# Optimization experiments

Measured on AMD Instinct MI355X. Metric: run time of the kernel, lower is better.

Reference implementation:

```python
import jax, jax.numpy as jnp
import numpy as np

EPS = 1e-6

def _log_g(x):
    # log of continuous g(x) = where(x>=0, x+0.5, sigmoid(x)) from minGRU paper
    return jnp.where(x >= 0, jnp.log(jax.nn.relu(x) + 0.5), -jax.nn.softplus(-x))

def setup_inputs() -> dict:
    key = jax.random.key(0)
    ks = jax.random.split(key, 4)
    B, S, D, E = 4, 2048, 1024, 8
    scale = D ** -0.5
    return {
        "inputs": jax.random.normal(ks[0], (B, S, D), dtype=jnp.float32),
        "norm_weight": jnp.ones((D,), jnp.float32),
        "router_w": jax.random.normal(ks[1], (E, D), jnp.float32) * scale,
        "router_b": jnp.zeros((E,), jnp.float32),
        "w_hg": jax.random.normal(ks[2], (E, 2 * D, D), jnp.float32) * scale,
        "w_out": jax.random.normal(ks[3], (E, D, D), jnp.float32) * scale,
    }

def reference(inputs, norm_weight, router_w, router_b, w_hg, w_out):
    D = inputs.shape[-1]
    # --- RMSNorm ---
    x = inputs * jax.lax.rsqrt(jnp.mean(inputs * inputs, axis=-1, keepdims=True) + EPS) * norm_weight
    # --- SMEAR: per-sample soft merge of expert weights via mean-pooled routing ---
    probs = jax.nn.softmax(jnp.mean(x, axis=1) @ router_w.T + router_b, axis=-1)  # [B,E]
    W_hg = jnp.einsum('be,ekd->bkd', probs, w_hg)    # [B,2D,D] merged to_hidden_and_gate
    W_out = jnp.einsum('be,eod->bod', probs, w_out)  # [B,D,D]  merged to_out
    # --- minGRU with merged weights (log-space parallel scan, no initial state) ---
    hg = jnp.einsum('bsd,bkd->bsk', x, W_hg)         # [B,S,2D]
    hidden, gate = hg[..., :D], hg[..., D:]
    log_coeffs = -jax.nn.softplus(gate)                      # log(1 - z_t)
    log_values = -jax.nn.softplus(-gate) + _log_g(hidden)    # log z_t + log g(h~_t)
    a_star = jnp.cumsum(log_coeffs, axis=1)
    log_h = a_star + jax.lax.cumlogsumexp(log_values - a_star, axis=1)
    h = jnp.exp(log_h)                               # [B,S,D] recurrent states
    new_state = h[:, -1:]                            # [B,1,D]
    out = jnp.einsum('bsk,bok->bso', h, W_out)       # proj_out
    aux_loss = jnp.zeros((), inputs.dtype)
    return (out + inputs, new_state, aux_loss)
```

## Files before the change

kernel.cpp:

```cpp
#include <hip/hip_runtime.h>
#include <hip/hip_bf16.h>
#include <hip/hip_fp16.h>

#define B_  4
#define S_  2048
#define D_  1024
#define E_  8
#define K2_ 2048

#define CHUNKS 64
#define CLEN   32

typedef __attribute__((ext_vector_type(8))) short short8;
typedef __attribute__((ext_vector_type(4))) float floatx4;

__device__ __forceinline__ void gld16(const void* g, const void* l) {
    __builtin_amdgcn_global_load_lds(
        (const __attribute__((address_space(1))) unsigned int*)g,
        (__attribute__((address_space(3))) unsigned int*)l, 16, 0, 0);
}

__device__ __forceinline__ unsigned short f2bf(float f) {
    unsigned int u = __float_as_uint(f);
    u += 0x7fffu + ((u >> 16) & 1u);
    return (unsigned short)(u >> 16);
}

__global__ void rmsnorm_k(const float* __restrict__ in, const float* __restrict__ nw,
                          __hip_bfloat16* __restrict__ x) {
    int b = blockIdx.y, s = blockIdx.x, t = threadIdx.x;
    const float4* row = (const float4*)(in + ((size_t)b * S_ + s) * D_);
    float4 v = row[t];
    float ss = v.x * v.x + v.y * v.y + v.z * v.z + v.w * v.w;
#pragma unroll
    for (int o = 32; o > 0; o >>= 1) ss += __shfl_down(ss, o, 64);
    __shared__ float ls[4];
    if ((t & 63) == 0) ls[t >> 6] = ss;
    __syncthreads();
    float tot = ls[0] + ls[1] + ls[2] + ls[3];
    float rs = rsqrtf(tot * (1.0f / (float)D_) + 1e-6f);
    float4 w = ((const float4*)nw)[t];
    ushort4 o;
    o.x = f2bf(v.x * rs * w.x); o.y = f2bf(v.y * rs * w.y);
    o.z = f2bf(v.z * rs * w.z); o.w = f2bf(v.w * rs * w.w);
    ((ushort4*)(x + ((size_t)b * S_ + s) * D_))[t] = o;
}

__global__ void xsum_k(const __hip_bfloat16* __restrict__ x, float* __restrict__ xs) {
    int d = blockIdx.x * 256 + threadIdx.x;
    int b = blockIdx.y;
    int s0 = blockIdx.z * 128;
    const __hip_bfloat16* p = x + ((size_t)b * S_ + s0) * D_ + d;
    float acc = 0.0f;
#pragma unroll 4
    for (int s = 0; s < 128; s++) { acc += __bfloat162float(*p); p += D_; }
    atomicAdd(&xs[b * D_ + d], acc);
}

__global__ void router_k(const float* __restrict__ xs, const float* __restrict__ rw,
                         const float* __restrict__ rb, float* __restrict__ probs,
                         float* __restrict__ aux) {
    int t = threadIdx.x;
    if (t == 255) *aux = 0.0f;
    int pair = t >> 3, sub = t & 7;
    int b = pair >> 3, e = pair & 7;
    float acc = 0.0f;
    for (int d = sub; d < D_; d += 8) acc += xs[b * D_ + d] * rw[e * D_ + d];
#pragma unroll
    for (int o = 4; o > 0; o >>= 1) acc += __shfl_down(acc, o, 8);
    __shared__ float lg[32];
    if (sub == 0) lg[pair] = acc * (1.0f / (float)S_) + rb[e];
    __syncthreads();
    if (t < 4) {
        float m = -1e30f;
        for (int e2 = 0; e2 < 8; e2++) m = fmaxf(m, lg[t * 8 + e2]);
        float ssum = 0.0f; float ex[8];
        for (int e2 = 0; e2 < 8; e2++) { ex[e2] = expf(lg[t * 8 + e2] - m); ssum += ex[e2]; }
        for (int e2 = 0; e2 < 8; e2++) probs[t * 8 + e2] = ex[e2] / ssum;
    }
}

__global__ void mix_k(const float* __restrict__ probs, const float* __restrict__ whg_e,
                      const float* __restrict__ wout_e, __hip_bfloat16* __restrict__ Whg,
                      __hip_bfloat16* __restrict__ Wout) {
    __shared__ float P[32];
    int t = threadIdx.x;
    if (t < 32) P[t] = probs[t];
    __syncthreads();
    size_t i4 = (size_t)blockIdx.x * 256 + t;
    const size_t T1q = (size_t)K2_ * D_ / 4;
    const size_t T2q = (size_t)D_ * D_ / 4;
    float4 a0 = {0,0,0,0}, a1 = {0,0,0,0}, a2 = {0,0,0,0}, a3 = {0,0,0,0};
    if (i4 < T1q) {
        const float4* src = (const float4*)whg_e;
#pragma unroll
        for (int e = 0; e < 8; e++) {
            float4 wv = src[(size_t)e * T1q + i4];
            float p0 = P[e], p1 = P[8 + e], p2 = P[16 + e], p3 = P[24 + e];
            a0.x += p0 * wv.x; a0.y += p0 * wv.y; a0.z += p0 * wv.z; a0.w += p0 * wv.w;
            a1.x += p1 * wv.x; a1.y += p1 * wv.y; a1.z += p1 * wv.z; a1.w += p1 * wv.w;
            a2.x += p2 * wv.x; a2.y += p2 * wv.y; a2.z += p2 * wv.z; a2.w += p2 * wv.w;
            a3.x += p3 * wv.x; a3.y += p3 * wv.y; a3.z += p3 * wv.z; a3.w += p3 * wv.w;
        }
        ushort4* dst = (ushort4*)Whg;
        ushort4 o;
        o.x = f2bf(a0.x); o.y = f2bf(a0.y); o.z = f2bf(a0.z); o.w = f2bf(a0.w);
        dst[0 * T1q + i4] = o;
        o.x = f2bf(a1.x); o.y = f2bf(a1.y); o.z = f2bf(a1.z); o.w = f2bf(a1.w);
        dst[1 * T1q + i4] = o;
        o.x = f2bf(a2.x); o.y = f2bf(a2.y); o.z = f2bf(a2.z); o.w = f2bf(a2.w);
        dst[2 * T1q + i4] = o;
        o.x = f2bf(a3.x); o.y = f2bf(a3.y); o.z = f2bf(a3.z); o.w = f2bf(a3.w);
        dst[3 * T1q + i4] = o;
    } else {
        size_t j4 = i4 - T1q;
        const float4* src = (const float4*)wout_e;
#pragma unroll
        for (int e = 0; e < 8; e++) {
            float4 wv = src[(size_t)e * T2q + j4];
            float p0 = P[e], p1 = P[8 + e], p2 = P[16 + e], p3 = P[24 + e];
            a0.x += p0 * wv.x; a0.y += p0 * wv.y; a0.z += p0 * wv.z; a0.w += p0 * wv.w;
            a1.x += p1 * wv.x; a1.y += p1 * wv.y; a1.z += p1 * wv.z; a1.w += p1 * wv.w;
            a2.x += p2 * wv.x; a2.y += p2 * wv.y; a2.z += p2 * wv.z; a2.w += p2 * wv.w;
            a3.x += p3 * wv.x; a3.y += p3 * wv.y; a3.z += p3 * wv.z; a3.w += p3 * wv.w;
        }
        ushort4* dst = (ushort4*)Wout;
        ushort4 o;
        o.x = f2bf(a0.x); o.y = f2bf(a0.y); o.z = f2bf(a0.z); o.w = f2bf(a0.w);
        dst[0 * T2q + j4] = o;
        o.x = f2bf(a1.x); o.y = f2bf(a1.y); o.z = f2bf(a1.z); o.w = f2bf(a1.w);
        dst[1 * T2q + j4] = o;
        o.x = f2bf(a2.x); o.y = f2bf(a2.y); o.z = f2bf(a2.z); o.w = f2bf(a2.w);
        dst[2 * T2q + j4] = o;
        o.x = f2bf(a3.x); o.y = f2bf(a3.y); o.z = f2bf(a3.z); o.w = f2bf(a3.w);
        dst[3 * T2q + j4] = o;
    }
}

__global__ __launch_bounds__(256) void gemm_hg_cv(
    const __hip_bfloat16* __restrict__ A, const __hip_bfloat16* __restrict__ Bm,
    __half2* __restrict__ cv) {
    const int K = D_;
    int bz = blockIdx.z;
    A  += (size_t)bz * S_ * D_;
    Bm += (size_t)bz * K2_ * D_;
    __half2* CV = cv + (size_t)bz * S_ * D_;
    int m0 = blockIdx.y * 128, n0 = blockIdx.x * 64;
    __shared__ __hip_bfloat16 lA[128][64];
    __shared__ __hip_bfloat16 lBh[64][64];
    __shared__ __hip_bfloat16 lBg[64][64];
    int t = threadIdx.x;
    int w = t >> 6, lane = t & 63;
    int lm = lane & 15, quad = lane >> 4;
    int wr = w >> 1, wc = w & 1;
    floatx4 acch[4][2] = {};
    floatx4 accg[4][2] = {};
    int srow = lane >> 3;
    int swzb = ((lane & 7) ^ srow) * 16;

    const __hip_bfloat16* Bh = Bm;
    const __hip_bfloat16* Bg = Bm + (size_t)D_ * K;

    for (int k0 = 0; k0 < K; k0 += 64) {
#pragma unroll
        for (int it = 0; it < 4; it++) {
            int r0 = (w * 4 + it) * 8;
            gld16((const char*)(A + (size_t)(m0 + r0 + srow) * K + k0) + swzb,
                  &lA[r0][0]);
        }
#pragma unroll
        for (int it = 0; it < 2; it++) {
            int r0 = (w * 2 + it) * 8;
            gld16((const char*)(Bh + (size_t)(n0 + r0 + srow) * K + k0) + swzb,
                  &lBh[r0][0]);
            gld16((const char*)(Bg + (size_t)(n0 + r0 + srow) * K + k0) + swzb,
                  &lBg[r0][0]);
        }
        __syncthreads();
#pragma unroll
        for (int kk = 0; kk < 64; kk += 32) {
            short8 af[4], bh[2], bg[2];
            int p = (((kk >> 3) + quad) ^ (lm & 7)) * 8;
#pragma unroll
            for (int i = 0; i < 4; i++)
                af[i] = *(const short8*)(&lA[wr * 64 + i * 16 + lm][p]);
#pragma unroll
            for (int j = 0; j < 2; j++) {
                bh[j] = *(const short8*)(&lBh[wc * 32 + j * 16 + lm][p]);
                bg[j] = *(const short8*)(&lBg[wc * 32 + j * 16 + lm][p]);
            }
#pragma unroll
            for (int i = 0; i < 4; i++)
#pragma unroll
                for (int j = 0; j < 2; j++) {
                    acch[i][j] = __builtin_amdgcn_mfma_f32_16x16x32_bf16(
                        af[i], bh[j], acch[i][j], 0, 0, 0);
                    accg[i][j] = __builtin_amdgcn_mfma_f32_16x16x32_bf16(
                        af[i], bg[j], accg[i][j], 0, 0, 0);
                }
        }
        __syncthreads();
    }
#pragma unroll
    for (int i = 0; i < 4; i++) {
#pragma unroll
        for (int j = 0; j < 2; j++) {
#pragma unroll
            for (int r = 0; r < 4; r++) {
                int m = m0 + wr * 64 + i * 16 + quad * 4 + r;
                int n = n0 + wc * 32 + j * 16 + lm;
                float hid = acch[i][j][r];
                float g   = accg[i][j][r];
                float c  = 1.0f / (1.0f + expf(g));
                float sg = 1.0f / (1.0f + expf(-g));
                float gfn = (hid >= 0.0f) ? (hid + 0.5f)
                                          : (1.0f / (1.0f + expf(-hid)));
                CV[(size_t)m * D_ + n] = __floats2half2_rn(c, sg * gfn);
            }
        }
    }
}

#define TM 128
#define TN 128
#define TBK 64
__global__ __launch_bounds__(256) void gemm_bf16_bt(
    const __hip_bfloat16* __restrict__ A, const __hip_bfloat16* __restrict__ Bm,
    float* __restrict__ C, const float* __restrict__ R,
    int M, int N, int K, size_t sa, size_t sb, size_t sc, size_t sr) {
    int bz = blockIdx.z;
    A += (size_t)bz * sa; Bm += (size_t)bz * sb; C += (size_t)bz * sc;
    if (R) R += (size_t)bz * sr;
    int m0 = blockIdx.y * TM, n0 = blockIdx.x * TN;
    __shared__ __hip_bfloat16 lA[TM][TBK];
    __shared__ __hip_bfloat16 lB[TN][TBK];
    int t = threadIdx.x;
    int w = t >> 6, lane = t & 63;
    int lm = lane & 15, quad = lane >> 4;
    int wr = w >> 1, wc = w & 1;
    floatx4 acc[4][4] = {};
    int srow = lane >> 3;
    int swzb = ((lane & 7) ^ srow) * 16;

    for (int k0 = 0; k0 < K; k0 += TBK) {
#pragma unroll
        for (int it = 0; it < 4; it++) {
            int r0 = (w * 4 + it) * 8;
            gld16((const char*)(A + (size_t)(m0 + r0 + srow) * K + k0) + swzb,
                  &lA[r0][0]);
            gld16((const char*)(Bm + (size_t)(n0 + r0 + srow) * K + k0) + swzb,
                  &lB[r0][0]);
        }
        __syncthreads();
#pragma unroll
        for (int kk = 0; kk < TBK; kk += 32) {
            short8 af[4], bf[4];
            int p = (((kk >> 3) + quad) ^ (lm & 7)) * 8;
#pragma unroll
            for (int i = 0; i < 4; i++)
                af[i] = *(const short8*)(&lA[wr * 64 + i * 16 + lm][p]);
#pragma unroll
            for (int j = 0; j < 4; j++)
                bf[j] = *(const short8*)(&lB[wc * 64 + j * 16 + lm][p]);
#pragma unroll
            for (int i = 0; i < 4; i++)
#pragma unroll
                for (int j = 0; j < 4; j++)
                    acc[i][j] = __builtin_amdgcn_mfma_f32_16x16x32_bf16(
                        af[i], bf[j], acc[i][j], 0, 0, 0);
        }
        __syncthreads();
    }
#pragma unroll
    for (int i = 0; i < 4; i++) {
#pragma unroll
        for (int j = 0; j < 4; j++) {
#pragma unroll
            for (int r = 0; r < 4; r++) {
                int m = m0 + wr * 64 + i * 16 + quad * 4 + r;
                int n = n0 + wc * 64 + j * 16 + lm;
                float v = acc[i][j][r];
                if (R) v += R[(size_t)m * N + n];
                C[(size_t)m * N + n] = v;
            }
        }
    }
}

__global__ void scanA_k(const __half2* __restrict__ cv, float* __restrict__ Cc,
                        float* __restrict__ Vc) {
    int c = blockIdx.x, b = blockIdx.y, t = threadIdx.x;
    const float4* p = (const float4*)(cv + (size_t)(b * S_ + c * CLEN) * D_) + t;
    float P0 = 1, P1 = 1, P2 = 1, P3 = 1;
    float V0 = 0, V1 = 0, V2 = 0, V3 = 0;
#pragma unroll 4
    for (int s = 0; s < CLEN; s++) {
        float4 raw = p[(size_t)s * (D_ / 4)];
        const __half2* e = (const __half2*)&raw;
        float c0 = __low2float(e[0]), v0 = __high2float(e[0]);
        float c1 = __low2float(e[1]), v1 = __high2float(e[1]);
        float c2 = __low2float(e[2]), v2 = __high2float(e[2]);
        float c3 = __low2float(e[3]), v3 = __high2float(e[3]);
        P0 *= c0; V0 = fmaf(c0, V0, v0);
        P1 *= c1; V1 = fmaf(c1, V1, v1);
        P2 *= c2; V2 = fmaf(c2, V2, v2);
        P3 *= c3; V3 = fmaf(c3, V3, v3);
    }
    size_t q = ((size_t)(b * CHUNKS + c)) * (D_ / 4) + t;
    ((float4*)Cc)[q] = make_float4(P0, P1, P2, P3);
    ((float4*)Vc)[q] = make_float4(V0, V1, V2, V3);
}

__global__ void scanC_k(const __half2* __restrict__ cv, const float* __restrict__ Cc,
                        const float* __restrict__ Vc,
                        __hip_bfloat16* __restrict__ hout, float* __restrict__ ns) {
    int c = blockIdx.x, b = blockIdx.y, t = threadIdx.x;
    float h0 = 0, h1 = 0, h2 = 0, h3 = 0;
#pragma unroll 4
    for (int cc = 0; cc < c; cc++) {
        size_t q = ((size_t)(b * CHUNKS + cc)) * (D_ / 4) + t;
        float4 C4 = ((const float4*)Cc)[q];
        float4 V4 = ((const float4*)Vc)[q];
        h0 = fmaf(C4.x, h0, V4.x); h1 = fmaf(C4.y, h1, V4.y);
        h2 = fmaf(C4.z, h2, V4.z); h3 = fmaf(C4.w, h3, V4.w);
    }
    const float4* p = (const float4*)(cv + (size_t)(b * S_ + c * CLEN) * D_) + t;
    ushort4* hq = (ushort4*)(hout + (size_t)(b * S_ + c * CLEN) * D_) + t;
#pragma unroll 4
    for (int s = 0; s < CLEN; s++) {
        float4 raw = p[(size_t)s * (D_ / 4)];
        const __half2* e = (const __half2*)&raw;
        h0 = fmaf(__low2float(e[0]), h0, __high2float(e[0]));
        h1 = fmaf(__low2float(e[1]), h1, __high2float(e[1]));
        h2 = fmaf(__low2float(e[2]), h2, __high2float(e[2]));
        h3 = fmaf(__low2float(e[3]), h3, __high2float(e[3]));
        ushort4 o;
        o.x = f2bf(h0); o.y = f2bf(h1); o.z = f2bf(h2); o.w = f2bf(h3);
        hq[(size_t)s * (D_ / 4)] = o;
    }
    if (c == CHUNKS - 1)
        ((float4*)(ns + (size_t)b * D_))[t] = make_float4(h0, h1, h2, h3);
}

extern "C" void kernel_launch(void* const* d_in, const int* in_sizes, int n_in,
                              void* d_out_v, int out_size, void* d_ws, size_t ws_size,
                              hipStream_t stream) {
    const float* inputs = (const float*)d_in[0];
    const float* nw     = (const float*)d_in[1];
    const float* rw     = (const float*)d_in[2];
    const float* rb     = (const float*)d_in[3];
    const float* whg_e  = (const float*)d_in[4];
    const float* wout_e = (const float*)d_in[5];
    float* out = (float*)d_out_v;

    float* ws = (float*)d_ws;
    __half2*        cv      = (__half2*)ws;
    __hip_bfloat16* x_bf    = (__hip_bfloat16*)(ws + 8388608);
    __hip_bfloat16* h_bf    = (__hip_bfloat16*)(ws + 12582912);
    __hip_bfloat16* Whg_bf  = (__hip_bfloat16*)(ws + 16777216);
    __hip_bfloat16* Wout_bf = (__hip_bfloat16*)(ws + 20971520);
    float* xsum  = ws + 23068672;
    float* probs = ws + 23072768;
    float* Cc    = ws + 23072800;
    float* Vc    = ws + 23334944;

    hipMemsetAsync(xsum, 0, (size_t)B_ * D_ * sizeof(float), stream);

    rmsnorm_k<<<dim3(S_, B_), 256, 0, stream>>>(inputs, nw, x_bf);
    xsum_k<<<dim3(D_ / 256, B_, 16), 256, 0, stream>>>(x_bf, xsum);
    router_k<<<1, 256, 0, stream>>>(xsum, rw, rb, probs,
                                    out + (size_t)B_ * S_ * D_ + (size_t)B_ * D_);
    mix_k<<<3072, 256, 0, stream>>>(probs, whg_e, wout_e, Whg_bf, Wout_bf);

    gemm_hg_cv<<<dim3(D_ / 64, S_ / 128, B_), 256, 0, stream>>>(x_bf, Whg_bf, cv);

    scanA_k<<<dim3(CHUNKS, B_), 256, 0, stream>>>(cv, Cc, Vc);
    scanC_k<<<dim3(CHUNKS, B_), 256, 0, stream>>>(
        cv, Cc, Vc, h_bf, out + (size_t)B_ * S_ * D_);

    gemm_bf16_bt<<<dim3(D_ / TN, S_ / TM, B_), 256, 0, stream>>>(
        h_bf, Wout_bf, out, inputs, S_, D_, D_,
        (size_t)S_ * D_, (size_t)D_ * D_, (size_t)S_ * D_, (size_t)S_ * D_);
}
```

Before: 334.2 us.

## Double-buffer LDS tiles in both GEMMs to overlap global loads with MFMA

```diff
diff --git a/kernel.cpp b/kernel.cpp
--- a/kernel.cpp
+++ b/kernel.cpp
@@ -65,6 +65,7 @@
     int pair = t >> 3, sub = t & 7;
     int b = pair >> 3, e = pair & 7;
     float acc = 0.0f;
+#pragma unroll 8
     for (int d = sub; d < D_; d += 8) acc += xs[b * D_ + d] * rw[e * D_ + d];
 #pragma unroll
     for (int o = 4; o > 0; o >>= 1) acc += __shfl_down(acc, o, 8);
@@ -146,9 +147,9 @@
     Bm += (size_t)bz * K2_ * D_;
     __half2* CV = cv + (size_t)bz * S_ * D_;
     int m0 = blockIdx.y * 128, n0 = blockIdx.x * 64;
-    __shared__ __hip_bfloat16 lA[128][64];
-    __shared__ __hip_bfloat16 lBh[64][64];
-    __shared__ __hip_bfloat16 lBg[64][64];
+    __shared__ __hip_bfloat16 lA[2][128][64];
+    __shared__ __hip_bfloat16 lBh[2][64][64];
+    __shared__ __hip_bfloat16 lBg[2][64][64];
     int t = threadIdx.x;
     int w = t >> 6, lane = t & 63;
     int lm = lane & 15, quad = lane >> 4;
@@ -161,33 +162,44 @@
     const __hip_bfloat16* Bh = Bm;
     const __hip_bfloat16* Bg = Bm + (size_t)D_ * K;
 
-    for (int k0 = 0; k0 < K; k0 += 64) {
+    auto stage = [&](int bb, int k0) {
 #pragma unroll
         for (int it = 0; it < 4; it++) {
             int r0 = (w * 4 + it) * 8;
             gld16((const char*)(A + (size_t)(m0 + r0 + srow) * K + k0) + swzb,
-                  &lA[r0][0]);
+                  &lA[bb][r0][0]);
         }
 #pragma unroll
         for (int it = 0; it < 2; it++) {
             int r0 = (w * 2 + it) * 8;
             gld16((const char*)(Bh + (size_t)(n0 + r0 + srow) * K + k0) + swzb,
-                  &lBh[r0][0]);
+                  &lBh[bb][r0][0]);
             gld16((const char*)(Bg + (size_t)(n0 + r0 + srow) * K + k0) + swzb,
-                  &lBg[r0][0]);
-        }
-        __syncthreads();
+                  &lBg[bb][r0][0]);
+        }
+    };
+
+    stage(0, 0);
+    int cur = 0;
+    for (int k0 = 0; k0 < K; k0 += 64) {
+        if (k0 + 64 < K) {
+            stage(cur ^ 1, k0 + 64);
+            asm volatile("s_waitcnt vmcnt(8)" ::: "memory");
+        } else {
+            asm volatile("s_waitcnt vmcnt(0)" ::: "memory");
+        }
+        __builtin_amdgcn_s_barrier();
 #pragma unroll
         for (int kk = 0; kk < 64; kk += 32) {
             short8 af[4], bh[2], bg[2];
             int p = (((kk >> 3) + quad) ^ (lm & 7)) * 8;
 #pragma unroll
             for (int i = 0; i < 4; i++)
-                af[i] = *(const short8*)(&lA[wr * 64 + i * 16 + lm][p]);
+                af[i] = *(const short8*)(&lA[cur][wr * 64 + i * 16 + lm][p]);
 #pragma unroll
             for (int j = 0; j < 2; j++) {
-                bh[j] = *(const short8*)(&lBh[wc * 32 + j * 16 + lm][p]);
-                bg[j] = *(const short8*)(&lBg[wc * 32 + j * 16 + lm][p]);
+                bh[j] = *(const short8*)(&lBh[cur][wc * 32 + j * 16 + lm][p]);
+                bg[j] = *(const short8*)(&lBg[cur][wc * 32 + j * 16 + lm][p]);
             }
 #pragma unroll
             for (int i = 0; i < 4; i++)
@@ -199,7 +211,9 @@
                         af[i], bg[j], accg[i][j], 0, 0, 0);
                 }
         }
-        __syncthreads();
+        asm volatile("s_waitcnt lgkmcnt(0)" ::: "memory");
+        __builtin_amdgcn_s_barrier();
+        cur ^= 1;
     }
 #pragma unroll
     for (int i = 0; i < 4; i++) {
@@ -211,8 +225,9 @@
                 int n = n0 + wc * 32 + j * 16 + lm;
                 float hid = acch[i][j][r];
                 float g   = accg[i][j][r];
-                float c  = 1.0f / (1.0f + expf(g));
-                float sg = 1.0f / (1.0f + expf(-g));
+                float eg  = expf(g);
+                float c   = 1.0f / (1.0f + eg);
+                float sg  = 1.0f - c;
                 float gfn = (hid >= 0.0f) ? (hid + 0.5f)
                                           : (1.0f / (1.0f + expf(-hid)));
                 CV[(size_t)m * D_ + n] = __floats2half2_rn(c, sg * gfn);
@@ -232,8 +247,8 @@
     A += (size_t)bz * sa; Bm += (size_t)bz * sb; C += (size_t)bz * sc;
     if (R) R += (size_t)bz * sr;
     int m0 = blockIdx.y * TM, n0 = blockIdx.x * TN;
-    __shared__ __hip_bfloat16 lA[TM][TBK];
-    __shared__ __hip_bfloat16 lB[TN][TBK];
+    __shared__ __hip_bfloat16 lA[2][TM][TBK];
+    __shared__ __hip_bfloat16 lB[2][TN][TBK];
     int t = threadIdx.x;
     int w = t >> 6, lane = t & 63;
     int lm = lane & 15, quad = lane >> 4;
@@ -242,26 +257,37 @@
     int srow = lane >> 3;
     int swzb = ((lane & 7) ^ srow) * 16;
 
-    for (int k0 = 0; k0 < K; k0 += TBK) {
+    auto stage = [&](int bb, int k0) {
 #pragma unroll
         for (int it = 0; it < 4; it++) {
             int r0 = (w * 4 + it) * 8;
             gld16((const char*)(A + (size_t)(m0 + r0 + srow) * K + k0) + swzb,
-                  &lA[r0][0]);
+                  &lA[bb][r0][0]);
             gld16((const char*)(Bm + (size_t)(n0 + r0 + srow) * K + k0) + swzb,
-                  &lB[r0][0]);
-        }
-        __syncthreads();
+                  &lB[bb][r0][0]);
+        }
+    };
+
+    stage(0, 0);
+    int cur = 0;
+    for (int k0 = 0; k0 < K; k0 += TBK) {
+        if (k0 + TBK < K) {
+            stage(cur ^ 1, k0 + TBK);
+            asm volatile("s_waitcnt vmcnt(8)" ::: "memory");
+        } else {
+            asm volatile("s_waitcnt vmcnt(0)" ::: "memory");
+        }
+        __builtin_amdgcn_s_barrier();
 #pragma unroll
         for (int kk = 0; kk < TBK; kk += 32) {
             short8 af[4], bf[4];
             int p = (((kk >> 3) + quad) ^ (lm & 7)) * 8;
 #pragma unroll
             for (int i = 0; i < 4; i++)
-                af[i] = *(const short8*)(&lA[wr * 64 + i * 16 + lm][p]);
+                af[i] = *(const short8*)(&lA[cur][wr * 64 + i * 16 + lm][p]);
 #pragma unroll
             for (int j = 0; j < 4; j++)
-                bf[j] = *(const short8*)(&lB[wc * 64 + j * 16 + lm][p]);
+                bf[j] = *(const short8*)(&lB[cur][wc * 64 + j * 16 + lm][p]);
 #pragma unroll
             for (int i = 0; i < 4; i++)
 #pragma unroll
@@ -269,7 +295,9 @@
                     acc[i][j] = __builtin_amdgcn_mfma_f32_16x16x32_bf16(
                         af[i], bf[j], acc[i][j], 0, 0, 0);
         }
-        __syncthreads();
+        asm volatile("s_waitcnt lgkmcnt(0)" ::: "memory");
+        __builtin_amdgcn_s_barrier();
+        cur ^= 1;
     }
 #pragma unroll
     for (int i = 0; i < 4; i++) {
```

Result: faster. 309.5 us (-7.4%).
